# Kernel tuning notes

Hardware: AMD Instinct MI355X
Metric: run time of the kernel (lower is better)

The kernel has to match this reference:

```python
import jax, jax.numpy as jnp
import numpy as np

HIDDEN = 1024
B, S = 8, 2048

def setup_inputs() -> dict:
    key = jax.random.key(0)
    k1, k2, k3, k4 = jax.random.split(key, 4)
    gain = 1.2
    # xavier_uniform bound for square [H,H] weight
    bound = gain * np.sqrt(6.0 / (HIDDEN + HIDDEN))
    return {
        "hidden_states": jax.random.normal(k1, (B, S, HIDDEN), dtype=jnp.float32),
        "Wq": jax.random.uniform(k2, (HIDDEN, HIDDEN), jnp.float32, -bound, bound),
        "bq": jnp.zeros((HIDDEN,), jnp.float32),
        "Wv": jax.random.uniform(k3, (HIDDEN, HIDDEN), jnp.float32, -bound, bound),
        "bv": jnp.zeros((HIDDEN,), jnp.float32),
        "anomaly_matrix": jax.random.uniform(k4, (HIDDEN, HIDDEN), jnp.float32, -2.0, 2.0),
    }

def reference(hidden_states, Wq, bq, Wv, bv, anomaly_matrix):
    # input magnitude rescaling
    input_norm = jnp.linalg.norm(hidden_states, axis=-1, keepdims=True)  # [B,S,1]
    scaled = hidden_states / (input_norm + 1e-9)
    # torch nn.Linear: x @ W.T + b
    q = jnp.einsum('bsh,oh->bso', scaled, Wq) + bq  # [B,S,H]
    v = jnp.einsum('bsh,oh->bso', scaled, Wv) + bv  # [B,S,H]
    # bilinear anomaly score: q @ A, then q @ (qA)^T
    tq = jnp.einsum('bsh,hk->bsk', q, anomaly_matrix)  # [B,S,H]
    scores = jnp.einsum('bsh,bth->bst', q, tq) / jnp.sqrt(jnp.float32(HIDDEN))  # [B,S,S]
    probs = jax.nn.softmax(scores, axis=-1)
    # dropout is identity in eval mode
    ctx = jnp.einsum('bst,bth->bsh', probs, v)  # [B,S,H]
    return ctx * input_norm
```

## Files before the change

kernel.cpp:

```cpp
#include <hip/hip_runtime.h>
#include <cstdint>
#include <cstddef>

#define H 1024
#define BB 8
#define SS 2048
#define MROWS (BB*SS)

typedef float  f32x4 __attribute__((ext_vector_type(4)));
typedef short  s16x8 __attribute__((ext_vector_type(8)));
typedef unsigned short u16x4 __attribute__((ext_vector_type(4)));
typedef unsigned short u16x8 __attribute__((ext_vector_type(8)));

__device__ __forceinline__ float b2f(unsigned short u) {
  union { unsigned int i; float f; } x; x.i = ((unsigned int)u) << 16; return x.f;
}
__device__ __forceinline__ unsigned short f2b(float f) {
  union { float f; unsigned int i; } x; x.f = f;
  unsigned int r = x.i + 0x7FFFu + ((x.i >> 16) & 1u);
  return (unsigned short)(r >> 16);
}

typedef __attribute__((address_space(1))) unsigned int guint;
typedef __attribute__((address_space(3))) unsigned int luint;
__device__ __forceinline__ void gld_lds16(const void* g, void* l) {
  __builtin_amdgcn_global_load_lds((guint*)g, (luint*)l, 16, 0, 0);
}

__global__ void norms_cast(const float* __restrict__ X, unsigned short* __restrict__ Xs,
                           float* __restrict__ norms) {
  const int row  = blockIdx.x * 4 + (threadIdx.x >> 6);
  const int lane = threadIdx.x & 63;
  const float4* xr = (const float4*)(X + (size_t)row * H);
  float4 d[4]; float s = 0.f;
#pragma unroll
  for (int j = 0; j < 4; ++j) {
    d[j] = xr[lane + j * 64];
    s += d[j].x*d[j].x + d[j].y*d[j].y + d[j].z*d[j].z + d[j].w*d[j].w;
  }
#pragma unroll
  for (int o = 32; o; o >>= 1) s += __shfl_xor(s, o);
  const float nrm = sqrtf(s);
  const float inv = 1.f / (nrm + 1e-9f);
  if (lane == 0) norms[row] = nrm;
  unsigned short* xo = Xs + (size_t)row * H;
#pragma unroll
  for (int j = 0; j < 4; ++j) {
    u16x4 o4;
    o4[0] = f2b(d[j].x * inv); o4[1] = f2b(d[j].y * inv);
    o4[2] = f2b(d[j].z * inv); o4[3] = f2b(d[j].w * inv);
    *(u16x4*)(xo + (size_t)(lane + j * 64) * 4) = o4;
  }
}

__global__ void cast_f32_bf16(const float* __restrict__ in, unsigned short* __restrict__ out) {
  const size_t i = ((size_t)blockIdx.x * 256 + threadIdx.x) * 4;
  float4 d = *(const float4*)(in + i);
  u16x4 o; o[0] = f2b(d.x); o[1] = f2b(d.y); o[2] = f2b(d.z); o[3] = f2b(d.w);
  *(u16x4*)(out + i) = o;
}

__global__ void transpose_cast_f32(const float* __restrict__ in, unsigned short* __restrict__ out) {
  __shared__ float t[32][33];
  const int c0 = blockIdx.x * 32, r0 = blockIdx.y * 32;
  const int tx = threadIdx.x, ty = threadIdx.y;
#pragma unroll
  for (int j = 0; j < 4; ++j)
    t[ty + j * 8][tx] = in[(size_t)(r0 + ty + j * 8) * H + c0 + tx];
  __syncthreads();
#pragma unroll
  for (int j = 0; j < 4; ++j)
    out[(size_t)(c0 + ty + j * 8) * H + r0 + tx] = f2b(t[tx][ty + j * 8]);
}

__global__ void transpose_bf16(const unsigned short* __restrict__ in, unsigned short* __restrict__ out) {
  __shared__ unsigned short t[32][33];
  const size_t zo = (size_t)blockIdx.z * SS * H;
  const int c0 = blockIdx.x * 32, r0 = blockIdx.y * 32;
  const int tx = threadIdx.x, ty = threadIdx.y;
#pragma unroll
  for (int j = 0; j < 4; ++j)
    t[ty + j * 8][tx] = in[zo + (size_t)(r0 + ty + j * 8) * H + c0 + tx];
  __syncthreads();
#pragma unroll
  for (int j = 0; j < 4; ++j)
    out[zo + (size_t)(c0 + ty + j * 8) * SS + r0 + tx] = t[tx][ty + j * 8];
}

template <int EPI>
__global__ __launch_bounds__(256, 2)
void gemm_nt(const unsigned short* __restrict__ A, int lda,
             const unsigned short* __restrict__ B0, int ldb, long sB,
             void* __restrict__ Cv, int ldc,
             const float* __restrict__ bias,
             const float* __restrict__ norms, const float* __restrict__ rs,
             int K) {
  __shared__ unsigned short Asm[128 * 64];
  __shared__ unsigned short Bsm[128 * 64];
  const int tid  = threadIdx.x;
  const int lane = tid & 63;
  const int w    = tid >> 6;
  const int bm = blockIdx.y, bn = blockIdx.x;
  const int b  = bm >> 4;
  const unsigned short* Ap = A  + (size_t)bm * 128 * lda;
  const unsigned short* Bp = B0 + (size_t)b * sB + (size_t)bn * 128 * ldb;

  const int st_row = w * 8 + (lane >> 3);
  const int st_col = ((lane & 7) ^ (lane >> 3)) * 8;
  const int lds_o  = w * 1024 + lane * 16;

  f32x4 acc[4][4] = {};
  const int wm = (w >> 1) * 64, wn = (w & 1) * 64;

  for (int k0 = 0; k0 < K; k0 += 64) {
#pragma unroll
    for (int c = 0; c < 4; ++c) {
      gld_lds16(Ap + (size_t)(c * 32 + st_row) * lda + k0 + st_col,
                (char*)Asm + c * 4096 + lds_o);
      gld_lds16(Bp + (size_t)(c * 32 + st_row) * ldb + k0 + st_col,
                (char*)Bsm + c * 4096 + lds_o);
    }
    __syncthreads();
#pragma unroll
    for (int ks = 0; ks < 2; ++ks) {
      s16x8 af[4], bfr[4];
#pragma unroll
      for (int i = 0; i < 4; ++i) {
        const int r  = wm + i * 16 + (lane & 15);
        const int cl = ks * 4 + (lane >> 4);
        af[i] = *(const s16x8*)((const char*)Asm + r * 128 + ((cl ^ (r & 7)) * 16));
      }
#pragma unroll
      for (int j = 0; j < 4; ++j) {
        const int r  = wn + j * 16 + (lane & 15);
        const int cl = ks * 4 + (lane >> 4);
        bfr[j] = *(const s16x8*)((const char*)Bsm + r * 128 + ((cl ^ (r & 7)) * 16));
      }
#pragma unroll
      for (int i = 0; i < 4; ++i)
#pragma unroll
        for (int j = 0; j < 4; ++j)
          acc[i][j] = __builtin_amdgcn_mfma_f32_16x16x32_bf16(af[i], bfr[j], acc[i][j], 0, 0, 0);
    }
    __syncthreads();
  }

  const int r0b = bm * 128 + wm + (lane >> 4) * 4;
  const int c0b = bn * 128 + wn + (lane & 15);
#pragma unroll
  for (int i = 0; i < 4; ++i) {
#pragma unroll
    for (int j = 0; j < 4; ++j) {
      const int c0 = c0b + j * 16;
#pragma unroll
      for (int r = 0; r < 4; ++r) {
        const int rr = r0b + i * 16 + r;
        const size_t idx = (size_t)rr * ldc + c0;
        const float val = acc[i][j][r];
        if constexpr (EPI == 0) {
          ((unsigned short*)Cv)[idx] = f2b(val + bias[c0]);
        } else if constexpr (EPI == 1) {
          ((unsigned short*)Cv)[idx] = f2b(val);
        } else if constexpr (EPI == 2) {
          ((unsigned short*)Cv)[idx] = f2b(val * 0.03125f);
        } else {
          ((float*)Cv)[idx] = val * norms[rr] * rs[rr];
        }
      }
    }
  }
}

__global__ void softmax_rows(unsigned short* __restrict__ S, float* __restrict__ rs) {
  const int row = blockIdx.x;
  const int tid = threadIdx.x, lane = tid & 63, w = tid >> 6;
  unsigned short* sr = S + (size_t)row * SS;
  u16x8 raw = *(const u16x8*)(sr + tid * 8);
  float v[8]; float m = -1e30f;
#pragma unroll
  for (int j = 0; j < 8; ++j) { v[j] = b2f(raw[j]); m = fmaxf(m, v[j]); }
#pragma unroll
  for (int o = 32; o; o >>= 1) m = fmaxf(m, __shfl_xor(m, o));
  __shared__ float mx[4], sm[4];
  if (lane == 0) mx[w] = m;
  __syncthreads();
  m = fmaxf(fmaxf(mx[0], mx[1]), fmaxf(mx[2], mx[3]));
  float s = 0.f;
#pragma unroll
  for (int j = 0; j < 8; ++j) { v[j] = __expf(v[j] - m); s += v[j]; }
#pragma unroll
  for (int o = 32; o; o >>= 1) s += __shfl_xor(s, o);
  if (lane == 0) sm[w] = s;
  __syncthreads();
  s = sm[0] + sm[1] + sm[2] + sm[3];
  u16x8 ow;
#pragma unroll
  for (int j = 0; j < 8; ++j) ow[j] = f2b(v[j]);
  *(u16x8*)(sr + tid * 8) = ow;
  if (tid == 0) rs[row] = 1.0f / s;
}

extern "C" void kernel_launch(void* const* d_in, const int* in_sizes, int n_in,
                              void* d_out, int out_size, void* d_ws, size_t ws_size,
                              hipStream_t stream) {
  (void)in_sizes; (void)n_in; (void)out_size; (void)ws_size;
  const float* X  = (const float*)d_in[0];
  const float* Wq = (const float*)d_in[1];
  const float* bq = (const float*)d_in[2];
  const float* Wv = (const float*)d_in[3];
  const float* bv = (const float*)d_in[4];
  const float* Am = (const float*)d_in[5];

  char* ws = (char*)d_ws;
  size_t off = 0;
  auto alloc = [&](size_t bytes) { char* p = ws + off; off += (bytes + 255) & ~255ull; return p; };
  float* norms          = (float*)alloc((size_t)MROWS * 4);
  float* rs             = (float*)alloc((size_t)MROWS * 4);
  unsigned short* Wqb   = (unsigned short*)alloc((size_t)H * H * 2);
  unsigned short* Wvb   = (unsigned short*)alloc((size_t)H * H * 2);
  unsigned short* Atb   = (unsigned short*)alloc((size_t)H * H * 2);
  unsigned short* Qb    = (unsigned short*)alloc((size_t)MROWS * H * 2);
  unsigned short* TQb   = (unsigned short*)alloc((size_t)MROWS * H * 2);
  unsigned short* VTb   = (unsigned short*)alloc((size_t)MROWS * H * 2);
  unsigned short* Xs    = (unsigned short*)alloc((size_t)MROWS * H * 2);
  unsigned short* Vb    = (unsigned short*)alloc((size_t)MROWS * H * 2);
  unsigned short* Sc    = Xs;

  norms_cast<<<MROWS / 4, 256, 0, stream>>>(X, Xs, norms);
  cast_f32_bf16<<<H * H / 1024, 256, 0, stream>>>(Wq, Wqb);
  cast_f32_bf16<<<H * H / 1024, 256, 0, stream>>>(Wv, Wvb);
  transpose_cast_f32<<<dim3(H / 32, H / 32), dim3(32, 8), 0, stream>>>(Am, Atb);
  gemm_nt<0><<<dim3(H / 128, MROWS / 128), 256, 0, stream>>>(Xs, H, Wqb, H, 0, Qb, H, bq, nullptr, nullptr, H);
  gemm_nt<0><<<dim3(H / 128, MROWS / 128), 256, 0, stream>>>(Xs, H, Wvb, H, 0, Vb, H, bv, nullptr, nullptr, H);
  transpose_bf16<<<dim3(H / 32, SS / 32, BB), dim3(32, 8), 0, stream>>>(Vb, VTb);
  gemm_nt<1><<<dim3(H / 128, MROWS / 128), 256, 0, stream>>>(Qb, H, Atb, H, 0, TQb, H, nullptr, nullptr, nullptr, H);
  gemm_nt<2><<<dim3(SS / 128, MROWS / 128), 256, 0, stream>>>(Qb, H, TQb, H, (long)SS * H, Sc, SS, nullptr, nullptr, nullptr, H);
  softmax_rows<<<MROWS, 256, 0, stream>>>(Sc, rs);
  gemm_nt<3><<<dim3(H / 128, MROWS / 128), 256, 0, stream>>>(Sc, SS, VTb, SS, (long)H * SS, d_out, H, nullptr, norms, rs, SS);
}
```

Measured before the change: 461.9 us.

## Rewrite bf16 GEMM with 256x256 tiles, 4-stage async LDS pipeline and block swizzle

The shared NT GEMM kernel now uses 512 threads and 256x256 output tiles with a K-step of 32. It adds a 4-deep ring of LDS buffers filled by direct global-to-LDS loads, with vmcnt waits so loads run ahead of the MFMA compute instead of a sync-load-compute loop. It also remaps block IDs into a grouped order for better L2 reuse, raises MFMA wave priority during compute, and hard-codes the K tile count per launch. The larger tiles cut operand re-reads, but each thread holds more accumulator registers and the grid is smaller, which lowers occupancy.

```diff
diff --git a/kernel.cpp b/kernel.cpp
--- a/kernel.cpp
+++ b/kernel.cpp
@@ -87,78 +87,92 @@
     out[zo + (size_t)(c0 + ty + j * 8) * SS + r0 + tx] = t[tx][ty + j * 8];
 }
 
-template <int EPI>
-__global__ __launch_bounds__(256, 2)
+template <int EPI, int TK>
+__global__ __launch_bounds__(512, 2)
 void gemm_nt(const unsigned short* __restrict__ A, int lda,
              const unsigned short* __restrict__ B0, int ldb, long sB,
              void* __restrict__ Cv, int ldc,
              const float* __restrict__ bias,
-             const float* __restrict__ norms, const float* __restrict__ rs,
-             int K) {
-  __shared__ unsigned short Asm[128 * 64];
-  __shared__ unsigned short Bsm[128 * 64];
-  const int tid  = threadIdx.x;
-  const int lane = tid & 63;
-  const int w    = tid >> 6;
-  const int bm = blockIdx.y, bn = blockIdx.x;
-  const int b  = bm >> 4;
-  const unsigned short* Ap = A  + (size_t)bm * 128 * lda;
-  const unsigned short* Bp = B0 + (size_t)b * sB + (size_t)bn * 128 * ldb;
-
-  const int st_row = w * 8 + (lane >> 3);
-  const int st_col = ((lane & 7) ^ (lane >> 3)) * 8;
-  const int lds_o  = w * 1024 + lane * 16;
-
-  f32x4 acc[4][4] = {};
-  const int wm = (w >> 1) * 64, wn = (w & 1) * 64;
-
-  for (int k0 = 0; k0 < K; k0 += 64) {
-#pragma unroll
-    for (int c = 0; c < 4; ++c) {
-      gld_lds16(Ap + (size_t)(c * 32 + st_row) * lda + k0 + st_col,
-                (char*)Asm + c * 4096 + lds_o);
-      gld_lds16(Bp + (size_t)(c * 32 + st_row) * ldb + k0 + st_col,
-                (char*)Bsm + c * 4096 + lds_o);
-    }
-    __syncthreads();
-#pragma unroll
-    for (int ks = 0; ks < 2; ++ks) {
-      s16x8 af[4], bfr[4];
-#pragma unroll
-      for (int i = 0; i < 4; ++i) {
-        const int r  = wm + i * 16 + (lane & 15);
-        const int cl = ks * 4 + (lane >> 4);
-        af[i] = *(const s16x8*)((const char*)Asm + r * 128 + ((cl ^ (r & 7)) * 16));
-      }
-#pragma unroll
-      for (int j = 0; j < 4; ++j) {
-        const int r  = wn + j * 16 + (lane & 15);
-        const int cl = ks * 4 + (lane >> 4);
-        bfr[j] = *(const s16x8*)((const char*)Bsm + r * 128 + ((cl ^ (r & 7)) * 16));
-      }
-#pragma unroll
-      for (int i = 0; i < 4; ++i)
-#pragma unroll
-        for (int j = 0; j < 4; ++j)
-          acc[i][j] = __builtin_amdgcn_mfma_f32_16x16x32_bf16(af[i], bfr[j], acc[i][j], 0, 0, 0);
-    }
-    __syncthreads();
-  }
-
-  const int r0b = bm * 128 + wm + (lane >> 4) * 4;
-  const int c0b = bn * 128 + wn + (lane & 15);
-#pragma unroll
-  for (int i = 0; i < 4; ++i) {
+             const float* __restrict__ norms, const float* __restrict__ rs) {
+  __shared__ __align__(16) unsigned short lds[4][2][256 * 32];
+  const int tid = threadIdx.x, lane = tid & 63, w = tid >> 6;
+
+  const int nx = gridDim.x;
+  int bid = blockIdx.y * nx + blockIdx.x;
+  bid = (bid & 7) * ((nx * (int)gridDim.y) >> 3) + (bid >> 3);
+  const int bn = bid % nx, bm = bid / nx;
+
+  const unsigned short* Ap = A  + (size_t)bm * 256 * lda;
+  const unsigned short* Bp = B0 + (size_t)(bm >> 3) * sB + (size_t)bn * 256 * ldb;
+
+  const int sr    = tid >> 2;
+  const int gslot = (tid & 3) ^ ((sr >> 1) & 3);
+  const unsigned short* As0 = Ap + (size_t)sr * lda + gslot * 8;
+  const unsigned short* Bs0 = Bp + (size_t)sr * ldb + gslot * 8;
+
+  auto STAGE = [&](int kt, int q) {
+    const unsigned short* as = As0 + kt * 32;
+    const unsigned short* bs = Bs0 + kt * 32;
+    unsigned short* la = &lds[q][0][0] + tid * 8;
+    unsigned short* lb = &lds[q][1][0] + tid * 8;
+    gld_lds16(as,                       la);
+    gld_lds16(as + (size_t)128 * lda,   la + 4096);
+    gld_lds16(bs,                       lb);
+    gld_lds16(bs + (size_t)128 * ldb,   lb + 4096);
+  };
+
+  const int wm = w >> 2, wn = w & 3;
+  const int rA = lane & 15;
+  const int ssw = ((lane >> 4) ^ ((rA >> 1) & 3)) * 8;
+  f32x4 acc[8][4] = {};
+
+  auto COMPUTE = [&](int t) {
+    const unsigned short* pa = &lds[t & 3][0][0] + (size_t)(wm * 128 + rA) * 32 + ssw;
+    const unsigned short* pb = &lds[t & 3][1][0] + (size_t)(wn * 64  + rA) * 32 + ssw;
+    s16x8 af[8], bf[4];
+#pragma unroll
+    for (int i = 0; i < 8; ++i) af[i] = *(const s16x8*)(pa + i * 512);
+#pragma unroll
+    for (int j = 0; j < 4; ++j) bf[j] = *(const s16x8*)(pb + j * 512);
+    __builtin_amdgcn_s_setprio(1);
+#pragma unroll
+    for (int i = 0; i < 8; ++i)
+#pragma unroll
+      for (int j = 0; j < 4; ++j)
+        acc[i][j] = __builtin_amdgcn_mfma_f32_16x16x32_bf16(af[i], bf[j], acc[i][j], 0, 0, 0);
+    __builtin_amdgcn_s_setprio(0);
+  };
+
+  STAGE(0, 0);
+  STAGE(1, 1);
+#pragma unroll 1
+  for (int t = 0; t < TK - 2; ++t) {
+    STAGE(t + 2, (t + 2) & 3);
+    asm volatile("s_waitcnt vmcnt(8)" ::: "memory");
+    __builtin_amdgcn_s_barrier();
+    COMPUTE(t);
+  }
+  asm volatile("s_waitcnt vmcnt(4)" ::: "memory");
+  __builtin_amdgcn_s_barrier();
+  COMPUTE(TK - 2);
+  asm volatile("s_waitcnt vmcnt(0)" ::: "memory");
+  __builtin_amdgcn_s_barrier();
+  COMPUTE(TK - 1);
+
+  const int r0b = bm * 256 + wm * 128 + (lane >> 4) * 4;
+  const int c0b = bn * 256 + wn * 64 + rA;
+#pragma unroll
+  for (int i = 0; i < 8; ++i) {
 #pragma unroll
     for (int j = 0; j < 4; ++j) {
-      const int c0 = c0b + j * 16;
+      const int cc = c0b + j * 16;
 #pragma unroll
       for (int r = 0; r < 4; ++r) {
         const int rr = r0b + i * 16 + r;
-        const size_t idx = (size_t)rr * ldc + c0;
+        const size_t idx = (size_t)rr * ldc + cc;
         const float val = acc[i][j][r];
         if constexpr (EPI == 0) {
-          ((unsigned short*)Cv)[idx] = f2b(val + bias[c0]);
+          ((unsigned short*)Cv)[idx] = f2b(val + bias[cc]);
         } else if constexpr (EPI == 1) {
           ((unsigned short*)Cv)[idx] = f2b(val);
         } else if constexpr (EPI == 2) {
@@ -230,11 +244,11 @@
   cast_f32_bf16<<<H * H / 1024, 256, 0, stream>>>(Wq, Wqb);
   cast_f32_bf16<<<H * H / 1024, 256, 0, stream>>>(Wv, Wvb);
   transpose_cast_f32<<<dim3(H / 32, H / 32), dim3(32, 8), 0, stream>>>(Am, Atb);
-  gemm_nt<0><<<dim3(H / 128, MROWS / 128), 256, 0, stream>>>(Xs, H, Wqb, H, 0, Qb, H, bq, nullptr, nullptr, H);
-  gemm_nt<0><<<dim3(H / 128, MROWS / 128), 256, 0, stream>>>(Xs, H, Wvb, H, 0, Vb, H, bv, nullptr, nullptr, H);
+  gemm_nt<0, 32><<<dim3(H / 256, MROWS / 256), 512, 0, stream>>>(Xs, H, Wqb, H, 0, Qb, H, bq, nullptr, nullptr);
+  gemm_nt<0, 32><<<dim3(H / 256, MROWS / 256), 512, 0, stream>>>(Xs, H, Wvb, H, 0, Vb, H, bv, nullptr, nullptr);
   transpose_bf16<<<dim3(H / 32, SS / 32, BB), dim3(32, 8), 0, stream>>>(Vb, VTb);
-  gemm_nt<1><<<dim3(H / 128, MROWS / 128), 256, 0, stream>>>(Qb, H, Atb, H, 0, TQb, H, nullptr, nullptr, nullptr, H);
-  gemm_nt<2><<<dim3(SS / 128, MROWS / 128), 256, 0, stream>>>(Qb, H, TQb, H, (long)SS * H, Sc, SS, nullptr, nullptr, nullptr, H);
+  gemm_nt<1, 32><<<dim3(H / 256, MROWS / 256), 512, 0, stream>>>(Qb, H, Atb, H, 0, TQb, H, nullptr, nullptr, nullptr);
+  gemm_nt<2, 32><<<dim3(SS / 256, MROWS / 256), 512, 0, stream>>>(Qb, H, TQb, H, (long)SS * H, Sc, SS, nullptr, nullptr, nullptr);
   softmax_rows<<<MROWS, 256, 0, stream>>>(Sc, rs);
-  gemm_nt<3><<<dim3(H / 128, MROWS / 128), 256, 0, stream>>>(Sc, SS, VTb, SS, (long)H * SS, d_out, H, nullptr, norms, rs, SS);
-}
+  gemm_nt<3, 64><<<dim3(H / 256, MROWS / 256), 512, 0, stream>>>(Sc, SS, VTb, SS, (long)H * SS, d_out, H, nullptr, norms, rs);
+}
```

New measurement: 408.0 us. 11.7% less time.
